# Optimization experiments

Measured on AMD Instinct MI355X. Metric: run time of the kernel, lower is better.

## Reference

```python
import jax, jax.numpy as jnp
import numpy as np

K = 3       # deformable kernel size
STRIDE = 2
PAD = 1


def conv2d(x, w, b, stride, pad):
    out = jax.lax.conv_general_dilated(
        x, w, (stride, stride), [(pad, pad), (pad, pad)],
        dimension_numbers=('NCHW', 'OIHW', 'NCHW'))
    return out + b[None, :, None, None]


def setup_inputs() -> dict:
    key = jax.random.key(0)
    ks = jax.random.split(key, 5)
    B, C, H, W, OC = 8, 64, 256, 256, 128
    x = jax.random.normal(ks[0], (B, C, H, W), jnp.float32)
    # offset conv: in_c -> 3*K*K, 3x3, stride 2, pad 1 (small weights ~ trained state)
    offset_w = jax.random.normal(ks[1], (3 * K * K, C, 3, 3), jnp.float32) * 0.05
    offset_b = jax.random.normal(ks[2], (3 * K * K,), jnp.float32) * 0.05
    # main deformable conv weight/bias
    weight = jax.random.normal(ks[3], (OC, C, K, K), jnp.float32) * (1.0 / np.sqrt(C * K * K))
    bias = jax.random.normal(ks[4], (OC,), jnp.float32) * 0.01
    return {'x': x, 'offset_w': offset_w, 'offset_b': offset_b, 'weight': weight, 'bias': bias}


def _bilinear_gather(img, py, px):
    # img: [C, H, W]; py/px: [K2, Ho, Wo] float sampling coords (zero padding outside)
    C, H, W = img.shape
    y0 = jnp.floor(py); x0 = jnp.floor(px)
    y1 = y0 + 1.0;      x1 = x0 + 1.0
    wy1 = py - y0; wy0 = 1.0 - wy1
    wx1 = px - x0; wx0 = 1.0 - wx1

    def corner(yc, xc, wgt):
        valid = (yc >= 0) & (yc <= H - 1) & (xc >= 0) & (xc <= W - 1)
        yi = jnp.clip(yc, 0, H - 1).astype(jnp.int32)
        xi = jnp.clip(xc, 0, W - 1).astype(jnp.int32)
        v = img[:, yi, xi]                      # [C, K2, Ho, Wo]
        return v * (wgt * valid)[None]

    return (corner(y0, x0, wy0 * wx0) + corner(y0, x1, wy0 * wx1)
            + corner(y1, x0, wy1 * wx0) + corner(y1, x1, wy1 * wx1))


def reference(x, offset_w, offset_b, weight, bias):
    B, C, H, W = x.shape
    K2 = K * K
    # offset/mask branch (zero-initialized conv in original; random here = trained state)
    om = conv2d(x, offset_w, offset_b, STRIDE, PAD)       # [B, 3*K2, Ho, Wo]
    off_x, off_y, mask = jnp.split(om, 3, axis=1)         # chunk order from source
    mask = jax.nn.sigmoid(mask)                           # [B, K2, Ho, Wo]
    Ho, Wo = off_x.shape[2], off_x.shape[3]
    # base sampling grid: p0 (output pixel * stride - pad) + kernel point offset + learned offset
    hy = (jnp.arange(Ho) * STRIDE - PAD).astype(jnp.float32)
    wx = (jnp.arange(Wo) * STRIDE - PAD).astype(jnp.float32)
    ky, kx = jnp.meshgrid(jnp.arange(K), jnp.arange(K), indexing='ij')
    ky = ky.reshape(K2).astype(jnp.float32)
    kx = kx.reshape(K2).astype(jnp.float32)
    py = off_y + ky[None, :, None, None] + hy[None, None, :, None]  # [B, K2, Ho, Wo]
    px = off_x + kx[None, :, None, None] + wx[None, None, None, :]
    # bilinear gather per batch element -> [B, C, K2, Ho, Wo]
    sampled = jax.vmap(_bilinear_gather)(x, py, px)
    sampled = sampled * mask[:, None]                     # mask modulation
    w = weight.reshape(weight.shape[0], C, K2)
    out = jnp.einsum('bckhw,ock->bohw', sampled, w) + bias[None, :, None, None]
    return out
```

## Files before the change

### kernel.cpp

```cpp
#include <hip/hip_runtime.h>

typedef unsigned short u16;
typedef __attribute__((ext_vector_type(8))) short bf16x8;
typedef __attribute__((ext_vector_type(8))) unsigned short u16x8;
typedef __attribute__((ext_vector_type(4))) float f32x4;
typedef __attribute__((ext_vector_type(2))) float f32x2;

#define HI 256
#define WI 256
#define CI 64
#define OC 128
#define HO 128
#define WO 128
#define NB 8
#define KC 576
#define KCP 584
#define TW 32

static __device__ __forceinline__ u16 f2bf(float f) {
    union { float f; unsigned u; } v; v.f = f;
    return (u16)((v.u + 0x7FFFu + ((v.u >> 16) & 1u)) >> 16);
}
static __device__ __forceinline__ float bf2f(u16 h) {
    union { unsigned u; float f; } v; v.u = ((unsigned)h) << 16;
    return v.f;
}
static __device__ __forceinline__ f32x2 unpack2(unsigned d) {
    union { unsigned u; float f; } lo, hi;
    lo.u = d << 16;
    hi.u = d & 0xffff0000u;
    f32x2 r; r.x = lo.f; r.y = hi.f;
    return r;
}

__global__ __launch_bounds__(256) void k_wconv(const float* __restrict__ w,
                                               const float* __restrict__ ow,
                                               u16* __restrict__ wbf, u16* __restrict__ wob) {
    int i = blockIdx.x * 256 + threadIdx.x;
    const int NW = OC * KCP;
    if (i < NW) {
        int oc = i / KCP, kc = i - oc * KCP;
        float v = 0.f;
        if (kc < KC) { int k = kc >> 6, c = kc & 63; v = w[oc * KC + c * 9 + k]; }
        wbf[i] = f2bf(v);
    } else {
        int i2 = i - NW;
        if (i2 < 32 * KCP) {
            int oc = i2 / KCP, kc = i2 - oc * KCP;
            float v = 0.f;
            if (oc < 27 && kc < KC) { int k = kc >> 6, c = kc & 63; v = ow[(oc * CI + c) * 9 + k]; }
            wob[i2] = f2bf(v);
        }
    }
}

__global__ __launch_bounds__(256) void k_tr(const float* __restrict__ x, u16* __restrict__ xT, int b0) {
    __shared__ u16 tile[64 * 68];
    const int t = threadIdx.x;
    const int w0 = blockIdx.x * 64;
    const int h  = blockIdx.y;
    const int bz = blockIdx.z;
    const float* xp = x + ((size_t)(b0 + bz) * CI) * (HI * WI) + h * WI + w0;
    #pragma unroll
    for (int i = 0; i < 4; ++i) {
        int c = i * 16 + (t >> 4);
        int w = (t & 15) * 4;
        float4 v = *(const float4*)(xp + (size_t)c * (HI * WI) + w);
        tile[(w + 0) * 68 + c] = f2bf(v.x);
        tile[(w + 1) * 68 + c] = f2bf(v.y);
        tile[(w + 2) * 68 + c] = f2bf(v.z);
        tile[(w + 3) * 68 + c] = f2bf(v.w);
    }
    __syncthreads();
    u16* op = xT + (size_t)bz * (HI * WI * CI) + ((size_t)h * WI + w0) * CI;
    #pragma unroll
    for (int j = 0; j < 4; ++j) {
        int w = j * 16 + (t >> 4);
        int c = (t & 15) * 4;
        *(ushort4*)(op + (size_t)w * CI + c) = *(const ushort4*)&tile[w * 68 + c];
    }
}

__global__ __launch_bounds__(256) void k_off(const u16* __restrict__ xT,
                                             const u16* __restrict__ wob,
                                             const float* __restrict__ ob,
                                             float* __restrict__ om) {
    __shared__ u16 s[32 * KCP];
    __shared__ int atab[288];
    __shared__ float red[2][2][64][4];
    const int t = threadIdx.x;
    const unsigned L = (blockIdx.z * gridDim.y + blockIdx.y) * gridDim.x + blockIdx.x;
    const unsigned nwg = gridDim.x * gridDim.y * gridDim.z;
    const unsigned W = (L & 7u) * (nwg >> 3) + (L >> 3);
    const int wo0 = (W & 3u) * 32;
    const int ho  = (W >> 2) & 127u;
    const int bz  = W >> 9;
    const u16* xb = xT + (size_t)bz * (HI * WI * CI);

    for (int p = t; p < 288; p += 256) {
        int px = p / 9, k = p - px * 9;
        int ky = k / 3, kx = k - ky * 3;
        int y  = ho * 2 - 1 + ky;
        int xx = (wo0 + px) * 2 - 1 + kx;
        bool valid = ((unsigned)y < HI) && ((unsigned)xx < WI);
        atab[p] = valid ? (y * WI + xx) * CI : -1;
    }
    __syncthreads();

    #pragma unroll 3
    for (int it = 0; it < 9; ++it) {
        int idx = it * 256 + t;
        int p = idx >> 3, c8 = idx & 7;
        int a = atab[p];
        u16x8 v = {0, 0, 0, 0, 0, 0, 0, 0};
        if (a >= 0) v = *(const u16x8*)(xb + a + c8 * 8);
        int px = p / 9, k = p - px * 9;
        *(u16x8*)&s[px * KCP + k * 64 + c8 * 8] = v;
    }
    __syncthreads();

    const int lane = t & 63, wv = t >> 6;
    const int q = lane >> 4, l15 = lane & 15;
    const int ph = wv & 1, kh = wv >> 1;
    const u16* sp  = &s[(ph * 16 + l15) * KCP + kh * 288 + q * 8];
    const u16* wp0 = wob + l15 * KCP + kh * 288 + q * 8;
    const u16* wp1 = wob + (16 + l15) * KCP + kh * 288 + q * 8;
    f32x4 acc0 = {0.f, 0.f, 0.f, 0.f}, acc1 = {0.f, 0.f, 0.f, 0.f};
    #pragma unroll
    for (int kt = 0; kt < 9; ++kt) {
        bf16x8 a  = *(const bf16x8*)(sp  + kt * 32);
        bf16x8 b0 = *(const bf16x8*)(wp0 + kt * 32);
        bf16x8 b1 = *(const bf16x8*)(wp1 + kt * 32);
        acc0 = __builtin_amdgcn_mfma_f32_16x16x32_bf16(a, b0, acc0, 0, 0, 0);
        acc1 = __builtin_amdgcn_mfma_f32_16x16x32_bf16(a, b1, acc1, 0, 0, 0);
    }
    if (kh == 1) {
        #pragma unroll
        for (int r = 0; r < 4; ++r) { red[ph][0][lane][r] = acc0[r]; red[ph][1][lane][r] = acc1[r]; }
    }
    __syncthreads();
    if (kh == 0) {
        #pragma unroll
        for (int r = 0; r < 4; ++r) { acc0[r] += red[ph][0][lane][r]; acc1[r] += red[ph][1][lane][r]; }
        const int wo = wo0 + ph * 16 + q * 4;
        float bv0 = ob[l15];
        float* o0 = om + ((size_t)(bz * 27 + l15) * HO + ho) * WO + wo;
        *(float4*)o0 = make_float4(acc0[0] + bv0, acc0[1] + bv0, acc0[2] + bv0, acc0[3] + bv0);
        if (l15 < 11) {
            float bv1 = ob[16 + l15];
            float* o1 = om + ((size_t)(bz * 27 + 16 + l15) * HO + ho) * WO + wo;
            *(float4*)o1 = make_float4(acc1[0] + bv1, acc1[1] + bv1, acc1[2] + bv1, acc1[3] + bv1);
        }
    }
}

__global__ __launch_bounds__(512, 6) void k_main(const u16* __restrict__ xT,
                                                 const float* __restrict__ om,
                                                 const u16* __restrict__ wbf,
                                                 const float* __restrict__ bias,
                                                 float* __restrict__ out, int b0) {
    __shared__ u16 s[TW * KCP];
    __shared__ int4   lav[288];
    __shared__ float4 lwv[288];

    const int t = threadIdx.x;
    const unsigned L = (blockIdx.z * gridDim.y + blockIdx.y) * gridDim.x + blockIdx.x;
    const unsigned nwg = gridDim.x * gridDim.y * gridDim.z;
    const unsigned W = (L & 7u) * (nwg >> 3) + (L >> 3);
    const int wo0 = (W & 3u) * TW;
    const int ho  = (W >> 2) & 127u;
    const int bz  = W >> 9;
    const int b = b0 + bz;

    if (t < 288) {
        const int p = t;
        const int px_id = p / 9, k = p - px_id * 9;
        const int wo = wo0 + px_id;
        const size_t base = ((size_t)bz * 27) * (HO * WO) + ho * WO + wo;
        float oxv = om[base + (size_t)k * (HO * WO)];
        float oyv = om[base + (size_t)(9 + k) * (HO * WO)];
        float omm = om[base + (size_t)(18 + k) * (HO * WO)];
        float m = 1.f / (1.f + __expf(-omm));
        float py  = oyv + (float)(k / 3) + (float)(ho * 2 - 1);
        float pxf = oxv + (float)(k % 3) + (float)(wo * 2 - 1);
        float fy = floorf(py), fx = floorf(pxf);
        float wy1 = py - fy, wx1 = pxf - fx;
        float wy0 = 1.f - wy1, wx0 = 1.f - wx1;
        int y0 = (int)fy, x0i = (int)fx;
        int y1 = y0 + 1, x1i = x0i + 1;
        bool vy0 = (y0 >= 0) && (y0 < HI), vy1 = (y1 >= 0) && (y1 < HI);
        bool vx0 = (x0i >= 0) && (x0i < WI), vx1 = (x1i >= 0) && (x1i < WI);
        float w00 = (vy0 && vx0) ? wy0 * wx0 * m : 0.f;
        float w01 = (vy0 && vx1) ? wy0 * wx1 * m : 0.f;
        float w10 = (vy1 && vx0) ? wy1 * wx0 * m : 0.f;
        float w11 = (vy1 && vx1) ? wy1 * wx1 * m : 0.f;
        int y0c = (y0 < 0 ? 0 : (y0 > HI-1 ? HI-1 : y0));
        int y1c = (y1 < 0 ? 0 : (y1 > HI-1 ? HI-1 : y1));
        int x0c = (x0i < 0 ? 0 : (x0i > WI-1 ? WI-1 : x0i));
        int x1c = (x1i < 0 ? 0 : (x1i > WI-1 ? WI-1 : x1i));
        lwv[p] = make_float4(w00, w01, w10, w11);
        lav[p] = make_int4((y0c * WI + x0c) * CI, (y0c * WI + x1c) * CI,
                           (y1c * WI + x0c) * CI, (y1c * WI + x1c) * CI);
    }
    __syncthreads();

    const u16* xb = xT + (size_t)bz * (HI * WI * CI);
    auto gb = [&](int i) {
        int p = i >> 3;
        int co = (i & 7) * 8;
        int px_id = p / 9, k = p - px_id * 9;
        float4 wv = lwv[p];
        int4   av = lav[p];
        uint4 da = *(const uint4*)(xb + av.x + co);
        uint4 db = *(const uint4*)(xb + av.y + co);
        uint4 dc = *(const uint4*)(xb + av.z + co);
        uint4 dd = *(const uint4*)(xb + av.w + co);
        const unsigned* ua = (const unsigned*)&da;
        const unsigned* ub = (const unsigned*)&db;
        const unsigned* uc = (const unsigned*)&dc;
        const unsigned* ud = (const unsigned*)&dd;
        union { u16x8 v; unsigned u[4]; } r;
        #pragma unroll
        for (int j2 = 0; j2 < 4; ++j2) {
            f32x2 e = wv.x * unpack2(ua[j2]);
            e += wv.y * unpack2(ub[j2]);
            e += wv.z * unpack2(uc[j2]);
            e += wv.w * unpack2(ud[j2]);
            unsigned pk;
            asm("v_cvt_pk_bf16_f32 %0, %1, %2" : "=v"(pk) : "v"(e.x), "v"(e.y));
            r.u[j2] = pk;
        }
        *(u16x8*)&s[px_id * KCP + k * 64 + co] = r.v;
    };
    #pragma unroll 2
    for (int it = 0; it < 4; ++it) gb(it * 512 + t);
    if (t < 256) gb(2048 + t);
    __syncthreads();

    const int lane = t & 63, wv_ = t >> 6;
    const int q = lane >> 4, l15 = lane & 15;
    const int ph = wv_ >> 2, og = wv_ & 3;
    const u16* sp  = &s[(ph * 16 + l15) * KCP + q * 8];
    const int oc0 = og * 32 + l15;
    const int oc1 = oc0 + 16;
    const u16* wp0 = wbf + oc0 * KCP + q * 8;
    const u16* wp1 = wbf + oc1 * KCP + q * 8;
    f32x4 acc0 = {0.f, 0.f, 0.f, 0.f};
    f32x4 acc1 = {0.f, 0.f, 0.f, 0.f};
    bf16x8 b0b[2], b1b[2];
    b0b[0] = *(const bf16x8*)(wp0);
    b1b[0] = *(const bf16x8*)(wp1);
    b0b[1] = *(const bf16x8*)(wp0 + 32);
    b1b[1] = *(const bf16x8*)(wp1 + 32);
    #pragma unroll
    for (int kt = 0; kt < 18; ++kt) {
        bf16x8 a = *(const bf16x8*)(sp + kt * 32);
        acc0 = __builtin_amdgcn_mfma_f32_16x16x32_bf16(a, b0b[kt & 1], acc0, 0, 0, 0);
        acc1 = __builtin_amdgcn_mfma_f32_16x16x32_bf16(a, b1b[kt & 1], acc1, 0, 0, 0);
        if (kt + 2 < 18) {
            b0b[kt & 1] = *(const bf16x8*)(wp0 + (kt + 2) * 32);
            b1b[kt & 1] = *(const bf16x8*)(wp1 + (kt + 2) * 32);
        }
    }
    const float bi0 = bias[oc0], bi1 = bias[oc1];
    const int wo = wo0 + ph * 16 + q * 4;
    float* op0 = out + (((size_t)b * OC + oc0) * HO + ho) * WO + wo;
    float* op1 = out + (((size_t)b * OC + oc1) * HO + ho) * WO + wo;
    *(float4*)op0 = make_float4(acc0[0] + bi0, acc0[1] + bi0, acc0[2] + bi0, acc0[3] + bi0);
    *(float4*)op1 = make_float4(acc1[0] + bi1, acc1[1] + bi1, acc1[2] + bi1, acc1[3] + bi1);
}

extern "C" void kernel_launch(void* const* d_in, const int* in_sizes, int n_in,
                              void* d_out, int out_size, void* d_ws, size_t ws_size,
                              hipStream_t stream) {
    const float* x        = (const float*)d_in[0];
    const float* offset_w = (const float*)d_in[1];
    const float* offset_b = (const float*)d_in[2];
    const float* weight   = (const float*)d_in[3];
    const float* bias     = (const float*)d_in[4];
    float* out = (float*)d_out;

    const size_t xT_full = (size_t)NB * HI * WI * CI * 2;
    const size_t om_full = (size_t)NB * 27 * HO * WO * 4;
    const size_t xT_b    = (size_t)HI * WI * CI * 2;
    const size_t om_b    = (size_t)27 * HO * WO * 4;
    const size_t wsz     = (size_t)(OC + 32) * KCP * 2;
    const int nwb = (int)(((OC + 32) * KCP + 255) / 256);

    if (ws_size >= xT_full + om_full + wsz) {
        u16*   xT  = (u16*)d_ws;
        float* om  = (float*)((char*)d_ws + xT_full);
        u16*   wbf = (u16*)((char*)d_ws + xT_full + om_full);
        u16*   wob = wbf + OC * KCP;
        hipLaunchKernelGGL(k_wconv, dim3(nwb), dim3(256), 0, stream, weight, offset_w, wbf, wob);
        hipLaunchKernelGGL(k_tr,   dim3(4, 256, NB), dim3(256), 0, stream, x, xT, 0);
        hipLaunchKernelGGL(k_off,  dim3(4, 128, NB), dim3(256), 0, stream, xT, wob, offset_b, om);
        hipLaunchKernelGGL(k_main, dim3(4, 128, NB), dim3(512), 0, stream, xT, om, wbf, bias, out, 0);
    } else {
        u16*   xT  = (u16*)d_ws;
        float* om  = (float*)((char*)d_ws + xT_b);
        u16*   wbf = (u16*)((char*)d_ws + xT_b + om_b);
        u16*   wob = wbf + OC * KCP;
        hipLaunchKernelGGL(k_wconv, dim3(nwb), dim3(256), 0, stream, weight, offset_w, wbf, wob);
        for (int b = 0; b < NB; ++b) {
            hipLaunchKernelGGL(k_tr,   dim3(4, 256, 1), dim3(256), 0, stream, x, xT, b);
            hipLaunchKernelGGL(k_off,  dim3(4, 128, 1), dim3(256), 0, stream, xT, wob, offset_b, om);
            hipLaunchKernelGGL(k_main, dim3(4, 128, 1), dim3(512), 0, stream, xT, om, wbf, bias, out, b);
        }
    }
}
```

Before: 364.2 us.

## Fuse offset conv kernel into main deformable conv kernel

Removes the separate k_off launch and computes the offset/mask convolution inside k_main for the same output tile. The result goes to global om and is read back after a barrier, so the launch and inter-kernel gap are removed while the om round trip stays, but now hits cache. Extra shared memory, a union buffer and more barriers reduce the launch-bounds occupancy hint from 6 to 4. Half the threads idle during the offset MFMA phase.

```diff
diff --git a/kernel.cpp b/kernel.cpp
--- a/kernel.cpp
+++ b/kernel.cpp
@@ -20,10 +20,6 @@
 static __device__ __forceinline__ u16 f2bf(float f) {
     union { float f; unsigned u; } v; v.f = f;
     return (u16)((v.u + 0x7FFFu + ((v.u >> 16) & 1u)) >> 16);
-}
-static __device__ __forceinline__ float bf2f(u16 h) {
-    union { unsigned u; float f; } v; v.u = ((unsigned)h) << 16;
-    return v.f;
 }
 static __device__ __forceinline__ f32x2 unpack2(unsigned d) {
     union { unsigned u; float f; } lo, hi;
@@ -81,87 +77,19 @@
     }
 }
 
-__global__ __launch_bounds__(256) void k_off(const u16* __restrict__ xT,
-                                             const u16* __restrict__ wob,
-                                             const float* __restrict__ ob,
-                                             float* __restrict__ om) {
-    __shared__ u16 s[32 * KCP];
-    __shared__ int atab[288];
-    __shared__ float red[2][2][64][4];
-    const int t = threadIdx.x;
-    const unsigned L = (blockIdx.z * gridDim.y + blockIdx.y) * gridDim.x + blockIdx.x;
-    const unsigned nwg = gridDim.x * gridDim.y * gridDim.z;
-    const unsigned W = (L & 7u) * (nwg >> 3) + (L >> 3);
-    const int wo0 = (W & 3u) * 32;
-    const int ho  = (W >> 2) & 127u;
-    const int bz  = W >> 9;
-    const u16* xb = xT + (size_t)bz * (HI * WI * CI);
-
-    for (int p = t; p < 288; p += 256) {
-        int px = p / 9, k = p - px * 9;
-        int ky = k / 3, kx = k - ky * 3;
-        int y  = ho * 2 - 1 + ky;
-        int xx = (wo0 + px) * 2 - 1 + kx;
-        bool valid = ((unsigned)y < HI) && ((unsigned)xx < WI);
-        atab[p] = valid ? (y * WI + xx) * CI : -1;
-    }
-    __syncthreads();
-
-    #pragma unroll 3
-    for (int it = 0; it < 9; ++it) {
-        int idx = it * 256 + t;
-        int p = idx >> 3, c8 = idx & 7;
-        int a = atab[p];
-        u16x8 v = {0, 0, 0, 0, 0, 0, 0, 0};
-        if (a >= 0) v = *(const u16x8*)(xb + a + c8 * 8);
-        int px = p / 9, k = p - px * 9;
-        *(u16x8*)&s[px * KCP + k * 64 + c8 * 8] = v;
-    }
-    __syncthreads();
-
-    const int lane = t & 63, wv = t >> 6;
-    const int q = lane >> 4, l15 = lane & 15;
-    const int ph = wv & 1, kh = wv >> 1;
-    const u16* sp  = &s[(ph * 16 + l15) * KCP + kh * 288 + q * 8];
-    const u16* wp0 = wob + l15 * KCP + kh * 288 + q * 8;
-    const u16* wp1 = wob + (16 + l15) * KCP + kh * 288 + q * 8;
-    f32x4 acc0 = {0.f, 0.f, 0.f, 0.f}, acc1 = {0.f, 0.f, 0.f, 0.f};
-    #pragma unroll
-    for (int kt = 0; kt < 9; ++kt) {
-        bf16x8 a  = *(const bf16x8*)(sp  + kt * 32);
-        bf16x8 b0 = *(const bf16x8*)(wp0 + kt * 32);
-        bf16x8 b1 = *(const bf16x8*)(wp1 + kt * 32);
-        acc0 = __builtin_amdgcn_mfma_f32_16x16x32_bf16(a, b0, acc0, 0, 0, 0);
-        acc1 = __builtin_amdgcn_mfma_f32_16x16x32_bf16(a, b1, acc1, 0, 0, 0);
-    }
-    if (kh == 1) {
-        #pragma unroll
-        for (int r = 0; r < 4; ++r) { red[ph][0][lane][r] = acc0[r]; red[ph][1][lane][r] = acc1[r]; }
-    }
-    __syncthreads();
-    if (kh == 0) {
-        #pragma unroll
-        for (int r = 0; r < 4; ++r) { acc0[r] += red[ph][0][lane][r]; acc1[r] += red[ph][1][lane][r]; }
-        const int wo = wo0 + ph * 16 + q * 4;
-        float bv0 = ob[l15];
-        float* o0 = om + ((size_t)(bz * 27 + l15) * HO + ho) * WO + wo;
-        *(float4*)o0 = make_float4(acc0[0] + bv0, acc0[1] + bv0, acc0[2] + bv0, acc0[3] + bv0);
-        if (l15 < 11) {
-            float bv1 = ob[16 + l15];
-            float* o1 = om + ((size_t)(bz * 27 + 16 + l15) * HO + ho) * WO + wo;
-            *(float4*)o1 = make_float4(acc1[0] + bv1, acc1[1] + bv1, acc1[2] + bv1, acc1[3] + bv1);
-        }
-    }
-}
-
-__global__ __launch_bounds__(512, 6) void k_main(const u16* __restrict__ xT,
-                                                 const float* __restrict__ om,
+__global__ __launch_bounds__(512, 4) void k_main(const u16* __restrict__ xT,
+                                                 const u16* __restrict__ wob,
                                                  const u16* __restrict__ wbf,
+                                                 const float* __restrict__ ob,
                                                  const float* __restrict__ bias,
+                                                 float* __restrict__ om,
                                                  float* __restrict__ out, int b0) {
     __shared__ u16 s[TW * KCP];
-    __shared__ int4   lav[288];
-    __shared__ float4 lwv[288];
+    __shared__ __align__(16) char ubuf[9216];
+    int*    atab = (int*)ubuf;
+    float*  red  = (float*)(ubuf + 1152);
+    int4*   lav  = (int4*)ubuf;
+    float4* lwv  = (float4*)(ubuf + 4608);
 
     const int t = threadIdx.x;
     const unsigned L = (blockIdx.z * gridDim.y + blockIdx.y) * gridDim.x + blockIdx.x;
@@ -171,6 +99,72 @@
     const int ho  = (W >> 2) & 127u;
     const int bz  = W >> 9;
     const int b = b0 + bz;
+    const u16* xb = xT + (size_t)bz * (HI * WI * CI);
+
+    if (t < 288) {
+        int p = t;
+        int px = p / 9, k = p - px * 9;
+        int ky = k / 3, kx = k - ky * 3;
+        int y  = ho * 2 - 1 + ky;
+        int xx = (wo0 + px) * 2 - 1 + kx;
+        bool valid = ((unsigned)y < HI) && ((unsigned)xx < WI);
+        atab[p] = valid ? (y * WI + xx) * CI : -1;
+    }
+    __syncthreads();
+
+    for (int idx = t; idx < 2304; idx += 512) {
+        int p = idx >> 3, c8 = idx & 7;
+        int a = atab[p];
+        u16x8 v = {0, 0, 0, 0, 0, 0, 0, 0};
+        if (a >= 0) v = *(const u16x8*)(xb + a + c8 * 8);
+        int px = p / 9, k = p - px * 9;
+        *(u16x8*)&s[px * KCP + k * 64 + c8 * 8] = v;
+    }
+    __syncthreads();
+
+    const int laneA = t & 63, wvA = (t >> 6) & 3;
+    const int qA = laneA >> 4, l15A = laneA & 15;
+    const int phA = wvA & 1, khA = wvA >> 1;
+    f32x4 accA0 = {0.f, 0.f, 0.f, 0.f}, accA1 = {0.f, 0.f, 0.f, 0.f};
+    if (t < 256) {
+        const u16* spA  = &s[(phA * 16 + l15A) * KCP + khA * 288 + qA * 8];
+        const u16* wpA0 = wob + l15A * KCP + khA * 288 + qA * 8;
+        const u16* wpA1 = wob + (16 + l15A) * KCP + khA * 288 + qA * 8;
+        #pragma unroll
+        for (int kt = 0; kt < 9; ++kt) {
+            bf16x8 a  = *(const bf16x8*)(spA  + kt * 32);
+            bf16x8 b0 = *(const bf16x8*)(wpA0 + kt * 32);
+            bf16x8 b1 = *(const bf16x8*)(wpA1 + kt * 32);
+            accA0 = __builtin_amdgcn_mfma_f32_16x16x32_bf16(a, b0, accA0, 0, 0, 0);
+            accA1 = __builtin_amdgcn_mfma_f32_16x16x32_bf16(a, b1, accA1, 0, 0, 0);
+        }
+        if (khA == 1) {
+            #pragma unroll
+            for (int r = 0; r < 4; ++r) {
+                red[((phA * 2 + 0) * 64 + laneA) * 4 + r] = accA0[r];
+                red[((phA * 2 + 1) * 64 + laneA) * 4 + r] = accA1[r];
+            }
+        }
+    }
+    __syncthreads();
+
+    if (t < 256 && khA == 0) {
+        #pragma unroll
+        for (int r = 0; r < 4; ++r) {
+            accA0[r] += red[((phA * 2 + 0) * 64 + laneA) * 4 + r];
+            accA1[r] += red[((phA * 2 + 1) * 64 + laneA) * 4 + r];
+        }
+        const int wo = wo0 + phA * 16 + qA * 4;
+        float bv0 = ob[l15A];
+        float* o0 = om + ((size_t)(bz * 27 + l15A) * HO + ho) * WO + wo;
+        *(float4*)o0 = make_float4(accA0[0] + bv0, accA0[1] + bv0, accA0[2] + bv0, accA0[3] + bv0);
+        if (l15A < 11) {
+            float bv1 = ob[16 + l15A];
+            float* o1 = om + ((size_t)(bz * 27 + 16 + l15A) * HO + ho) * WO + wo;
+            *(float4*)o1 = make_float4(accA1[0] + bv1, accA1[1] + bv1, accA1[2] + bv1, accA1[3] + bv1);
+        }
+    }
+    __syncthreads();
 
     if (t < 288) {
         const int p = t;
@@ -204,7 +198,6 @@
     }
     __syncthreads();
 
-    const u16* xb = xT + (size_t)bz * (HI * WI * CI);
     auto gb = [&](int i) {
         int p = i >> 3;
         int co = (i & 7) * 8;
@@ -294,8 +287,8 @@
         u16*   wob = wbf + OC * KCP;
         hipLaunchKernelGGL(k_wconv, dim3(nwb), dim3(256), 0, stream, weight, offset_w, wbf, wob);
         hipLaunchKernelGGL(k_tr,   dim3(4, 256, NB), dim3(256), 0, stream, x, xT, 0);
-        hipLaunchKernelGGL(k_off,  dim3(4, 128, NB), dim3(256), 0, stream, xT, wob, offset_b, om);
-        hipLaunchKernelGGL(k_main, dim3(4, 128, NB), dim3(512), 0, stream, xT, om, wbf, bias, out, 0);
+        hipLaunchKernelGGL(k_main, dim3(4, 128, NB), dim3(512), 0, stream,
+                           xT, wob, wbf, offset_b, bias, om, out, 0);
     } else {
         u16*   xT  = (u16*)d_ws;
         float* om  = (float*)((char*)d_ws + xT_b);
@@ -304,8 +297,8 @@
         hipLaunchKernelGGL(k_wconv, dim3(nwb), dim3(256), 0, stream, weight, offset_w, wbf, wob);
         for (int b = 0; b < NB; ++b) {
             hipLaunchKernelGGL(k_tr,   dim3(4, 256, 1), dim3(256), 0, stream, x, xT, b);
-            hipLaunchKernelGGL(k_off,  dim3(4, 128, 1), dim3(256), 0, stream, xT, wob, offset_b, om);
-            hipLaunchKernelGGL(k_main, dim3(4, 128, 1), dim3(512), 0, stream, xT, om, wbf, bias, out, b);
-        }
-    }
-}
+            hipLaunchKernelGGL(k_main, dim3(4, 128, 1), dim3(512), 0, stream,
+                               xT, wob, wbf, offset_b, bias, om, out, b);
+        }
+    }
+}
```

Result: no change. 364.9 us (+0.2%).
